# Performance work log

Measured on AMD Instinct MI355X. Metric: run time of the kernel, lower is better.

The kernel has to match this reference:

```python
import jax, jax.numpy as jnp
import numpy as np

B, N, DIM = 2, 2048, 2048
H, KVH, HD = 16, 4, 128
N_REP = H // KVH
SCALE = np.float32(HD ** -0.5)


def setup_inputs() -> dict:
    key = jax.random.key(0)
    ks = jax.random.split(key, 5)
    x = jax.random.normal(ks[0], (B, N, DIM), dtype=jnp.float32)
    mask = jnp.tril(jnp.ones((N, N), dtype=jnp.int32))[None, None]  # [1,1,N,N] causal
    Wq = jax.random.normal(ks[1], (DIM, H * HD), dtype=jnp.float32) * (DIM ** -0.5)
    Wk = jax.random.normal(ks[2], (DIM, KVH * HD), dtype=jnp.float32) * (DIM ** -0.5)
    Wv = jax.random.normal(ks[3], (DIM, KVH * HD), dtype=jnp.float32) * (DIM ** -0.5)
    Wo = jax.random.normal(ks[4], (H * HD, DIM), dtype=jnp.float32) * ((H * HD) ** -0.5)
    return {"x": x, "mask": mask, "Wq": Wq, "Wk": Wk, "Wv": Wv, "Wo": Wo}


def reference(x, mask, Wq, Wk, Wv, Wo):
    Bx, Nx, _ = x.shape
    # projections -> [B, heads, N, head_dim]
    q = (x @ Wq).reshape(Bx, Nx, H, HD).transpose(0, 2, 1, 3)
    k = (x @ Wk).reshape(Bx, Nx, KVH, HD).transpose(0, 2, 1, 3)
    v = (x @ Wv).reshape(Bx, Nx, KVH, HD).transpose(0, 2, 1, 3)
    # repeat_interleave KV heads to match query heads (GQA)
    k = jnp.repeat(k, N_REP, axis=1)
    v = jnp.repeat(v, N_REP, axis=1)
    attn = jnp.einsum('bhqd,bhkd->bhqk', q, k) * SCALE
    attn = jnp.where(mask == 0, jnp.float32(-jnp.inf), attn)
    attn = jax.nn.softmax(attn, axis=-1)
    out = jnp.einsum('bhqk,bhkd->bhqd', attn, v)
    out = out.transpose(0, 2, 1, 3).reshape(Bx, Nx, H * HD)
    return out @ Wo
```

## Files before the change

kernel.cpp:

```cpp
#include <hip/hip_runtime.h>
#include <hip/hip_bf16.h>
#include <math.h>

typedef __bf16 bf16;
typedef bf16 bf16x8 __attribute__((ext_vector_type(8)));
typedef bf16 bf16x4v __attribute__((ext_vector_type(4)));
typedef float f32x4 __attribute__((ext_vector_type(4)));

#define GLD16(g, l) __builtin_amdgcn_global_load_lds(                          \
    (__attribute__((address_space(1))) void*)(g),                              \
    (__attribute__((address_space(3))) void*)(l), 16, 0, 0)

#define MFMA16(a, b, c) __builtin_amdgcn_mfma_f32_16x16x32_bf16((a), (b), (c), 0, 0, 0)

#if __has_builtin(__builtin_amdgcn_exp2f)
#define EXP2F(x) __builtin_amdgcn_exp2f(x)
#else
#define EXP2F(x) exp2f(x)
#endif

__device__ __forceinline__ f32x4 shfl_xor4(f32x4 a, int m) {
  f32x4 r;
  #pragma unroll
  for (int i = 0; i < 4; i++) r[i] = __shfl_xor(a[i], m);
  return r;
}

__global__ __launch_bounds__(256) void prep(const float* __restrict__ x,
                                            const float* __restrict__ Wq,
                                            const float* __restrict__ Wk,
                                            const float* __restrict__ Wv,
                                            const float* __restrict__ Wo,
                                            bf16* __restrict__ Xb,
                                            bf16* __restrict__ Wqkvt,
                                            bf16* __restrict__ Wot,
                                            float qscale) {
  const int id = blockIdx.x;
  const int tid = threadIdx.x;
  if (id >= 10240) {
    int i = (id - 10240) * 256 + tid;
    float4 v = ((const float4*)x)[i];
    bf16x4v o;
    o.x = (bf16)v.x; o.y = (bf16)v.y; o.z = (bf16)v.z; o.w = (bf16)v.w;
    ((bf16x4v*)Xb)[i] = o;
    return;
  }
  __shared__ float t[32][33];
  const float* in; bf16* out; int colsIn, outRowOff, bx, by; float scale;
  if (id < 4096)      { in = Wq; out = Wqkvt; colsIn = 2048; outRowOff = 0;    scale = qscale; bx = id & 63;          by = id >> 6; }
  else if (id < 5120) { in = Wk; out = Wqkvt; colsIn = 512;  outRowOff = 2048; scale = 1.0f;   bx = (id - 4096) & 15; by = (id - 4096) >> 4; }
  else if (id < 6144) { in = Wv; out = Wqkvt; colsIn = 512;  outRowOff = 2560; scale = 1.0f;   bx = (id - 5120) & 15; by = (id - 5120) >> 4; }
  else                { in = Wo; out = Wot;   colsIn = 2048; outRowOff = 0;    scale = 1.0f;   bx = (id - 6144) & 63; by = (id - 6144) >> 6; }
  const int c0 = bx * 32, r0 = by * 32;
  const int tx = tid & 31, ty = tid >> 5;
  #pragma unroll
  for (int i = 0; i < 32; i += 8)
    t[ty + i][tx] = in[(size_t)(r0 + ty + i) * colsIn + (c0 + tx)];
  __syncthreads();
  #pragma unroll
  for (int i = 0; i < 32; i += 8)
    out[(size_t)(outRowOff + c0 + ty + i) * 2048 + (r0 + tx)] = (bf16)(t[tx][ty + i] * scale);
}

__global__ __launch_bounds__(256, 2) void gemm_bt(const bf16* __restrict__ A,
                                                  const bf16* __restrict__ Bt,
                                                  bf16* __restrict__ C,
                                                  bf16* __restrict__ Vg,
                                                  int N, int K) {
  __shared__ __attribute__((aligned(16))) bf16 As[128 * 32];
  __shared__ __attribute__((aligned(16))) bf16 Bs[128 * 32];
  const int tid = threadIdx.x;
  const int lane = tid & 63;
  const int wave = tid >> 6;
  const int wm = wave >> 1, wn = wave & 1;
  const int l15 = lane & 15, quad = lane >> 4;
  const int rowBase = blockIdx.y * 128;
  const int colBase = blockIdx.x * 128;

  f32x4 acc[4][4] = {};

  const int cb0 = wave * 64;
  const int c0 = cb0 + lane;
  const int c1 = c0 + 256;
  const bf16* a0 = A + (size_t)(rowBase + (c0 >> 2)) * K + (c0 & 3) * 8;
  const bf16* a1 = A + (size_t)(rowBase + (c1 >> 2)) * K + (c1 & 3) * 8;
  const bf16* b0 = Bt + (size_t)(colBase + (c0 >> 2)) * K + (c0 & 3) * 8;
  const bf16* b1 = Bt + (size_t)(colBase + (c1 >> 2)) * K + (c1 & 3) * 8;
  bf16* lA0 = &As[cb0 * 8];
  bf16* lA1 = &As[(cb0 + 256) * 8];
  bf16* lB0 = &Bs[cb0 * 8];
  bf16* lB1 = &Bs[(cb0 + 256) * 8];

  for (int k0 = 0; k0 < K; k0 += 32) {
    GLD16(a0 + k0, lA0);
    GLD16(a1 + k0, lA1);
    GLD16(b0 + k0, lB0);
    GLD16(b1 + k0, lB1);
    __syncthreads();
    bf16x8 af[4], bfr[4];
    #pragma unroll
    for (int i = 0; i < 4; i++)
      af[i] = *(const bf16x8*)&As[(wm * 64 + i * 16 + l15) * 32 + quad * 8];
    #pragma unroll
    for (int i = 0; i < 4; i++)
      bfr[i] = *(const bf16x8*)&Bs[(wn * 64 + i * 16 + l15) * 32 + quad * 8];
    #pragma unroll
    for (int i = 0; i < 4; i++)
      #pragma unroll
      for (int j = 0; j < 4; j++)
        acc[i][j] = MFMA16(af[i], bfr[j], acc[i][j]);
    __syncthreads();
  }

  if (colBase >= 2560) {
    const int kvh = (colBase - 2560) >> 7;
    #pragma unroll
    for (int i = 0; i < 4; i++) {
      int row = rowBase + wm * 64 + i * 16 + quad * 4;
      int bb = row >> 11;
      int n0 = row & 2047;
      #pragma unroll
      for (int j = 0; j < 4; j++) {
        int d = wn * 64 + j * 16 + l15;
        bf16x4v o;
        #pragma unroll
        for (int r = 0; r < 4; r++) o[r] = (bf16)acc[i][j][r];
        *(bf16x4v*)&Vg[((size_t)(bb * 4 + kvh) * 128 + d) * 2048 + n0] = o;
      }
    }
  } else {
    #pragma unroll
    for (int i = 0; i < 4; i++) {
      int row = rowBase + wm * 64 + i * 16 + quad * 4;
      #pragma unroll
      for (int j = 0; j < 4; j++) {
        int col = colBase + wn * 64 + j * 16 + l15;
        #pragma unroll
        for (int r = 0; r < 4; r++)
          C[(size_t)(row + r) * N + col] = (bf16)acc[i][j][r];
      }
    }
  }
}

__global__ __launch_bounds__(128, 2) void gemm_bt64(const bf16* __restrict__ A,
                                                    const bf16* __restrict__ Bt,
                                                    float* __restrict__ C,
                                                    int N, int K) {
  __shared__ __attribute__((aligned(16))) bf16 As[64 * 32];
  __shared__ __attribute__((aligned(16))) bf16 Bs[128 * 32];
  const int tid = threadIdx.x;
  const int lane = tid & 63;
  const int wave = tid >> 6;
  const int l15 = lane & 15, quad = lane >> 4;
  const int rowBase = blockIdx.y * 64;
  const int colBase = blockIdx.x * 128;

  f32x4 acc[4][4] = {};

  const bf16* aP[2]; bf16* lAp[2];
  #pragma unroll
  for (int p = 0; p < 2; p++) {
    int s = p * 128 + tid;
    aP[p] = A + (size_t)(rowBase + (s >> 2)) * K + (s & 3) * 8;
    lAp[p] = &As[(p * 128 + wave * 64) * 8];
  }
  const bf16* bP[4]; bf16* lBp[4];
  #pragma unroll
  for (int p = 0; p < 4; p++) {
    int s = p * 128 + tid;
    bP[p] = Bt + (size_t)(colBase + (s >> 2)) * K + (s & 3) * 8;
    lBp[p] = &Bs[(p * 128 + wave * 64) * 8];
  }

  for (int k0 = 0; k0 < K; k0 += 32) {
    #pragma unroll
    for (int p = 0; p < 2; p++) GLD16(aP[p] + k0, lAp[p]);
    #pragma unroll
    for (int p = 0; p < 4; p++) GLD16(bP[p] + k0, lBp[p]);
    __syncthreads();
    bf16x8 af[4], bfr[4];
    #pragma unroll
    for (int i = 0; i < 4; i++)
      af[i] = *(const bf16x8*)&As[(i * 16 + l15) * 32 + quad * 8];
    #pragma unroll
    for (int i = 0; i < 4; i++)
      bfr[i] = *(const bf16x8*)&Bs[(wave * 64 + i * 16 + l15) * 32 + quad * 8];
    #pragma unroll
    for (int i = 0; i < 4; i++)
      #pragma unroll
      for (int j = 0; j < 4; j++)
        acc[i][j] = MFMA16(af[i], bfr[j], acc[i][j]);
    __syncthreads();
  }

  #pragma unroll
  for (int i = 0; i < 4; i++) {
    int row = rowBase + i * 16 + quad * 4;
    #pragma unroll
    for (int j = 0; j < 4; j++) {
      int col = colBase + wave * 64 + j * 16 + l15;
      #pragma unroll
      for (int r = 0; r < 4; r++)
        C[(size_t)(row + r) * N + col] = acc[i][j][r];
    }
  }
}

#define MASKV (-1e30f)

__device__ const unsigned char BMAP[22] = {
  28, 58, 24, 50, 20, 46, 36, 32,
  62, 59, 54, 51, 47, 42, 55, 63,
  0, 4, 8, 12, 16, 43
};

#define SLOT_F32 16640

__global__ __launch_bounds__(256, 2) void gqa_attn(const bf16* __restrict__ QKV,
                                                   const bf16* __restrict__ Vg,
                                                   bf16* __restrict__ Obf,
                                                   float* __restrict__ Part) {
  __shared__ __attribute__((aligned(16))) bf16 Kl[64 * 128];
  __shared__ __attribute__((aligned(16))) bf16 Vt[128 * 64];
  __shared__ __attribute__((aligned(16))) bf16 Pl[4][32 * 68];

  const int tid = threadIdx.x;
  const int lane = tid & 63;
  const int wave = tid >> 6;
  const int l15 = lane & 15, quad = lane >> 4;

  const int e = BMAP[blockIdx.x >> 5];
  const int bh = blockIdx.x & 31;
  const int qt = e >> 2;
  const int split = (e >> 1) & 1;
  const int half = e & 1;
  const int b = bh >> 4, h = bh & 15, kvh = h >> 2;
  const int q0 = qt * 128;
  const int nkt = 2 * qt + 2;
  const int kt_lo = (split && half) ? (nkt >> 1) : 0;
  const int kt_hi = (split && !half) ? (nkt >> 1) : nkt;

  const size_t rs = 3072;
  const bf16* Qb  = QKV + (size_t)b * 2048 * rs + h * 128;
  const bf16* Kb  = QKV + (size_t)b * 2048 * rs + 2048 + kvh * 128;
  const bf16* Vgb = Vg + (size_t)(b * 4 + kvh) * 128 * 2048;

  bf16x8 qf[2][4];
  #pragma unroll
  for (int mt = 0; mt < 2; mt++) {
    int row = q0 + wave * 32 + mt * 16 + l15;
    #pragma unroll
    for (int ks = 0; ks < 4; ks++)
      qf[mt][ks] = *(const bf16x8*)&Qb[(size_t)row * rs + ks * 32 + quad * 8];
  }

  bf16x8 ones8;
  #pragma unroll
  for (int i = 0; i < 8; i++) ones8[i] = (bf16)1.0f;

  const bf16* kp[4]; const bf16* vp[4];
  bf16* kl[4]; bf16* vl[4];
  #pragma unroll
  for (int t = 0; t < 4; t++) {
    int keyl = wave * 16 + t * 4 + (lane >> 4);
    int ck = (lane & 15) ^ (4 * (t & 1) + (lane >> 4));
    kp[t] = Kb + (size_t)(kt_lo * 64 + keyl) * rs + ck * 8;
    kl[t] = &Kl[(wave * 16 + t * 4) * 128];
    int dl = wave * 32 + t * 8 + (lane >> 3);
    int cv = (lane & 7) ^ (lane >> 3);
    vp[t] = Vgb + (size_t)dl * 2048 + kt_lo * 64 + cv * 8;
    vl[t] = &Vt[(wave * 32 + t * 8) * 64];
  }

  f32x4 oacc[2][8] = {};
  f32x4 lacc[2] = {};
  f32x4 mrow[2];
  #pragma unroll
  for (int mt = 0; mt < 2; mt++)
    #pragma unroll
    for (int r = 0; r < 4; r++) mrow[mt][r] = MASKV;

  const int myrow_hi = q0 + wave * 32 + 31;
  for (int kt = kt_lo; kt < kt_hi; kt++) {
    const int k0 = kt * 64;
    __syncthreads();
    #pragma unroll
    for (int t = 0; t < 4; t++) { GLD16(kp[t], kl[t]); kp[t] += 64 * rs; }
    #pragma unroll
    for (int t = 0; t < 4; t++) { GLD16(vp[t], vl[t]); vp[t] += 64; }
    __syncthreads();

    if (k0 > myrow_hi) continue;

    f32x4 s[2][4] = {};
    #pragma unroll
    for (int ks = 0; ks < 4; ks++) {
      #pragma unroll
      for (int nt = 0; nt < 4; nt++) {
        bf16x8 kf = *(const bf16x8*)&Kl[(nt * 16 + l15) * 128 +
                                        (((ks * 4 + quad) ^ (l15 & 7)) * 8)];
        s[0][nt] = MFMA16(qf[0][ks], kf, s[0][nt]);
        s[1][nt] = MFMA16(qf[1][ks], kf, s[1][nt]);
      }
    }
    if (kt >= nkt - 2) {
      #pragma unroll
      for (int mt = 0; mt < 2; mt++) {
        int rowb = q0 + wave * 32 + mt * 16 + quad * 4;
        #pragma unroll
        for (int nt = 0; nt < 4; nt++) {
          int col = k0 + nt * 16 + l15;
          #pragma unroll
          for (int r = 0; r < 4; r++)
            if (col > rowb + r) s[mt][nt][r] = MASKV;
        }
      }
    }
    #pragma unroll
    for (int mt = 0; mt < 2; mt++) {
      f32x4 mx = s[mt][0];
      #pragma unroll
      for (int nt = 1; nt < 4; nt++)
        #pragma unroll
        for (int r = 0; r < 4; r++) mx[r] = fmaxf(mx[r], s[mt][nt][r]);
      #pragma unroll
      for (int d = 1; d < 16; d <<= 1) {
        f32x4 o = shfl_xor4(mx, d);
        #pragma unroll
        for (int r = 0; r < 4; r++) mx[r] = fmaxf(mx[r], o[r]);
      }
      bool noresc = (mx[0] <= mrow[mt][0] + 8.f) && (mx[1] <= mrow[mt][1] + 8.f) &&
                    (mx[2] <= mrow[mt][2] + 8.f) && (mx[3] <= mrow[mt][3] + 8.f);
      if (!__all(noresc)) {
        f32x4 alpha;
        #pragma unroll
        for (int r = 0; r < 4; r++) {
          float mn = fmaxf(mrow[mt][r], mx[r]);
          alpha[r] = EXP2F(mrow[mt][r] - mn);
          mrow[mt][r] = mn;
        }
        #pragma unroll
        for (int no = 0; no < 8; no++)
          #pragma unroll
          for (int r = 0; r < 4; r++) oacc[mt][no][r] *= alpha[r];
        #pragma unroll
        for (int r = 0; r < 4; r++) lacc[mt][r] *= alpha[r];
      }
      #pragma unroll
      for (int nt = 0; nt < 4; nt++)
        #pragma unroll
        for (int r = 0; r < 4; r++) {
          float p = EXP2F(s[mt][nt][r] - mrow[mt][r]);
          Pl[wave][(mt * 16 + quad * 4 + r) * 68 + nt * 16 + l15] = (bf16)p;
        }
    }
    #pragma unroll
    for (int ks2 = 0; ks2 < 2; ks2++) {
      bf16x8 pf0 = *(const bf16x8*)&Pl[wave][l15 * 68 + ks2 * 32 + quad * 8];
      bf16x8 pf1 = *(const bf16x8*)&Pl[wave][(16 + l15) * 68 + ks2 * 32 + quad * 8];
      lacc[0] = MFMA16(pf0, ones8, lacc[0]);
      lacc[1] = MFMA16(pf1, ones8, lacc[1]);
      #pragma unroll
      for (int no = 0; no < 8; no++) {
        bf16x8 vf = *(const bf16x8*)&Vt[(no * 16 + l15) * 64 +
                                        (((ks2 * 4 + quad) ^ (l15 & 7)) * 8)];
        oacc[0][no] = MFMA16(pf0, vf, oacc[0][no]);
        oacc[1][no] = MFMA16(pf1, vf, oacc[1][no]);
      }
    }
  }

  if (!split) {
    #pragma unroll
    for (int mt = 0; mt < 2; mt++) {
      f32x4 linv;
      #pragma unroll
      for (int r = 0; r < 4; r++) linv[r] = 1.0f / lacc[mt][r];
      int row = q0 + wave * 32 + mt * 16 + quad * 4;
      #pragma unroll
      for (int no = 0; no < 8; no++) {
        int col = h * 128 + no * 16 + l15;
        #pragma unroll
        for (int r = 0; r < 4; r++)
          Obf[(size_t)(b * 2048 + row + r) * 2048 + col] = (bf16)(oacc[mt][no][r] * linv[r]);
      }
    }
  } else {
    const int fidx = bh * 6 + (qt - 10);
    float* slot = Part + (size_t)(fidx * 2 + half) * SLOT_F32;
    #pragma unroll
    for (int mt = 0; mt < 2; mt++) {
      int row = wave * 32 + mt * 16 + quad * 4;
      #pragma unroll
      for (int no = 0; no < 8; no++) {
        int col = no * 16 + l15;
        #pragma unroll
        for (int r = 0; r < 4; r++)
          slot[(row + r) * 128 + col] = oacc[mt][no][r];
      }
    }
    if (l15 == 0) {
      #pragma unroll
      for (int mt = 0; mt < 2; mt++)
        #pragma unroll
        for (int r = 0; r < 4; r++) {
          int row = wave * 32 + mt * 16 + quad * 4 + r;
          slot[16384 + row] = mrow[mt][r];
          slot[16512 + row] = lacc[mt][r];
        }
    }
  }
}

__global__ __launch_bounds__(256) void merge_split(const float* __restrict__ Part,
                                                   bf16* __restrict__ Obf) {
  const int fidx = blockIdx.x;
  const int bh = fidx / 6, qt = 10 + fidx % 6;
  const int b = bh >> 4, h = bh & 15;
  const int tid = threadIdx.x;
  const int cl = (tid & 31) * 4;
  const int r0 = tid >> 5;
  const float* s0 = Part + (size_t)(fidx * 2) * SLOT_F32;
  const float* s1 = s0 + SLOT_F32;
  #pragma unroll
  for (int i = 0; i < 16; i++) {
    int row = r0 + i * 8;
    float m0 = s0[16384 + row], l0 = s0[16512 + row];
    float m1 = s1[16384 + row], l1 = s1[16512 + row];
    float ms = fmaxf(m0, m1);
    float a0 = EXP2F(m0 - ms), a1 = EXP2F(m1 - ms);
    float linv = 1.0f / (l0 * a0 + l1 * a1);
    f32x4 v0 = *(const f32x4*)&s0[row * 128 + cl];
    f32x4 v1 = *(const f32x4*)&s1[row * 128 + cl];
    bf16x4v o;
    #pragma unroll
    for (int r = 0; r < 4; r++) o[r] = (bf16)((v0[r] * a0 + v1[r] * a1) * linv);
    *(bf16x4v*)&Obf[(size_t)(b * 2048 + qt * 128 + row) * 2048 + h * 128 + cl] = o;
  }
}

extern "C" void kernel_launch(void* const* d_in, const int* in_sizes, int n_in,
                              void* d_out, int out_size, void* d_ws, size_t ws_size,
                              hipStream_t stream) {
  const float* x  = (const float*)d_in[0];
  const float* Wq = (const float*)d_in[2];
  const float* Wk = (const float*)d_in[3];
  const float* Wv = (const float*)d_in[4];
  const float* Wo = (const float*)d_in[5];
  float* out = (float*)d_out;

  bf16* Xb    = (bf16*)d_ws;
  bf16* Wqkvt = Xb + 8388608;
  bf16* Wot   = Wqkvt + 6291456;
  bf16* QKV   = Wot + 4194304;
  bf16* Obf   = QKV + 12582912;
  bf16* Vg    = Obf + 8388608;

  float* Part = (float*)d_ws;

  const float qscale = (float)(0.08838834764831845 * 1.4426950408889634);

  prep<<<18432, 256, 0, stream>>>(x, Wq, Wk, Wv, Wo, Xb, Wqkvt, Wot, qscale);
  gemm_bt<<<dim3(24, 32), 256, 0, stream>>>(Xb, Wqkvt, QKV, Vg, 3072, 2048);
  gqa_attn<<<704, 256, 0, stream>>>(QKV, Vg, Obf, Part);
  merge_split<<<192, 256, 0, stream>>>(Part, Obf);
  gemm_bt64<<<dim3(16, 64), 128, 0, stream>>>(Obf, Wot, out, 2048, 2048);
}
```

Baseline: 321.1 us.

## Switch attention to transposed 32x32 MFMA with register-resident P via permlane swap

Rewrites the attention inner loop to compute S^T with 32x32x16 MFMAs so each lane owns one query row. Softmax max and sum then need only a single cross-half shuffle, and P is packed to bf16 with v_cvt_pk and redistributed via v_permlane32_swap instead of a round trip through LDS. The row sum is accumulated in VALU rather than by an MFMA against ones, and occupancy is raised to 3 blocks per CU now that the P LDS buffer is gone. The cost is higher register pressure per lane under the tighter launch bound, plus reliance on gfx950-specific instructions.

Result: faster. 303.7 us (-5.4%).

```diff
diff --git a/kernel.cpp b/kernel.cpp
--- a/kernel.cpp
+++ b/kernel.cpp
@@ -6,12 +6,16 @@
 typedef bf16 bf16x8 __attribute__((ext_vector_type(8)));
 typedef bf16 bf16x4v __attribute__((ext_vector_type(4)));
 typedef float f32x4 __attribute__((ext_vector_type(4)));
+typedef float f32x16 __attribute__((ext_vector_type(16)));
+typedef unsigned int u32;
+typedef u32 u32x4 __attribute__((ext_vector_type(4)));
 
 #define GLD16(g, l) __builtin_amdgcn_global_load_lds(                          \
     (__attribute__((address_space(1))) void*)(g),                              \
     (__attribute__((address_space(3))) void*)(l), 16, 0, 0)
 
 #define MFMA16(a, b, c) __builtin_amdgcn_mfma_f32_16x16x32_bf16((a), (b), (c), 0, 0, 0)
+#define MFMA32(a, b, c) __builtin_amdgcn_mfma_f32_32x32x16_bf16((a), (b), (c), 0, 0, 0)
 
 #if __has_builtin(__builtin_amdgcn_exp2f)
 #define EXP2F(x) __builtin_amdgcn_exp2f(x)
@@ -19,11 +23,13 @@
 #define EXP2F(x) exp2f(x)
 #endif
 
-__device__ __forceinline__ f32x4 shfl_xor4(f32x4 a, int m) {
-  f32x4 r;
-  #pragma unroll
-  for (int i = 0; i < 4; i++) r[i] = __shfl_xor(a[i], m);
+__device__ __forceinline__ u32 cvtpk_bf16(float lo, float hi_) {
+  u32 r;
+  asm("v_cvt_pk_bf16_f32 %0, %1, %2" : "=v"(r) : "v"(lo), "v"(hi_));
   return r;
+}
+__device__ __forceinline__ void pl32swap(u32& a, u32& b) {
+  asm("v_permlane32_swap_b32 %0, %1" : "+v"(a), "+v"(b));
 }
 
 __global__ __launch_bounds__(256) void prep(const float* __restrict__ x,
@@ -217,18 +223,17 @@
 
 #define SLOT_F32 16640
 
-__global__ __launch_bounds__(256, 2) void gqa_attn(const bf16* __restrict__ QKV,
+__global__ __launch_bounds__(256, 3) void gqa_attn(const bf16* __restrict__ QKV,
                                                    const bf16* __restrict__ Vg,
                                                    bf16* __restrict__ Obf,
                                                    float* __restrict__ Part) {
   __shared__ __attribute__((aligned(16))) bf16 Kl[64 * 128];
   __shared__ __attribute__((aligned(16))) bf16 Vt[128 * 64];
-  __shared__ __attribute__((aligned(16))) bf16 Pl[4][32 * 68];
 
   const int tid = threadIdx.x;
   const int lane = tid & 63;
   const int wave = tid >> 6;
-  const int l15 = lane & 15, quad = lane >> 4;
+  const int l31 = lane & 31, hi = lane >> 5;
 
   const int e = BMAP[blockIdx.x >> 5];
   const int bh = blockIdx.x & 31;
@@ -246,18 +251,12 @@
   const bf16* Kb  = QKV + (size_t)b * 2048 * rs + 2048 + kvh * 128;
   const bf16* Vgb = Vg + (size_t)(b * 4 + kvh) * 128 * 2048;
 
-  bf16x8 qf[2][4];
-  #pragma unroll
-  for (int mt = 0; mt < 2; mt++) {
-    int row = q0 + wave * 32 + mt * 16 + l15;
-    #pragma unroll
-    for (int ks = 0; ks < 4; ks++)
-      qf[mt][ks] = *(const bf16x8*)&Qb[(size_t)row * rs + ks * 32 + quad * 8];
-  }
-
-  bf16x8 ones8;
-  #pragma unroll
-  for (int i = 0; i < 8; i++) ones8[i] = (bf16)1.0f;
+  const int qrow = q0 + wave * 32 + l31;
+
+  bf16x8 qf[8];
+  #pragma unroll
+  for (int hs = 0; hs < 8; hs++)
+    qf[hs] = *(const bf16x8*)&Qb[(size_t)qrow * rs + hs * 16 + hi * 8];
 
   const bf16* kp[4]; const bf16* vp[4];
   bf16* kl[4]; bf16* vl[4];
@@ -273,13 +272,9 @@
     vl[t] = &Vt[(wave * 32 + t * 8) * 64];
   }
 
-  f32x4 oacc[2][8] = {};
-  f32x4 lacc[2] = {};
-  f32x4 mrow[2];
-  #pragma unroll
-  for (int mt = 0; mt < 2; mt++)
-    #pragma unroll
-    for (int r = 0; r < 4; r++) mrow[mt][r] = MASKV;
+  f32x16 oacc[4] = {};
+  float lacc = 0.f;
+  float mrow = MASKV;
 
   const int myrow_hi = q0 + wave * 32 + 31;
   for (int kt = kt_lo; kt < kt_hi; kt++) {
@@ -293,122 +288,112 @@
 
     if (k0 > myrow_hi) continue;
 
-    f32x4 s[2][4] = {};
+    f32x16 sacc[2] = {};
+    #pragma unroll
+    for (int hs = 0; hs < 8; hs++) {
+      #pragma unroll
+      for (int kg = 0; kg < 2; kg++) {
+        bf16x8 kf = *(const bf16x8*)&Kl[(kg * 32 + l31) * 128 +
+                                        (((hs * 2 + hi) ^ (l31 & 7)) * 8)];
+        sacc[kg] = MFMA32(kf, qf[hs], sacc[kg]);
+      }
+    }
+    if (kt >= nkt - 2) {
+      #pragma unroll
+      for (int kg = 0; kg < 2; kg++)
+        #pragma unroll
+        for (int r = 0; r < 16; r++) {
+          int key = k0 + kg * 32 + (r & 3) + 8 * (r >> 2) + 4 * hi;
+          if (key > qrow) sacc[kg][r] = MASKV;
+        }
+    }
+    float mx = sacc[0][0];
+    #pragma unroll
+    for (int kg = 0; kg < 2; kg++)
+      #pragma unroll
+      for (int r = 0; r < 16; r++) mx = fmaxf(mx, sacc[kg][r]);
+    mx = fmaxf(mx, __shfl_xor(mx, 32));
+    bool noresc = (mx <= mrow + 8.f);
+    if (!__all(noresc)) {
+      float mn = fmaxf(mrow, mx);
+      float alpha = EXP2F(mrow - mn);
+      mrow = mn;
+      #pragma unroll
+      for (int dg = 0; dg < 4; dg++)
+        #pragma unroll
+        for (int r = 0; r < 16; r++) oacc[dg][r] *= alpha;
+      lacc *= alpha;
+    }
+    float ls = 0.f;
+    #pragma unroll
+    for (int kg = 0; kg < 2; kg++)
+      #pragma unroll
+      for (int r = 0; r < 16; r++) {
+        float p = (float)(bf16)EXP2F(sacc[kg][r] - mrow);
+        sacc[kg][r] = p;
+        ls += p;
+      }
+    ls += __shfl_xor(ls, 32);
+    lacc += ls;
+    u32 w[4][4];
+    #pragma unroll
+    for (int kg = 0; kg < 2; kg++) {
+      u32 A0 = cvtpk_bf16(sacc[kg][0], sacc[kg][1]);
+      u32 A1 = cvtpk_bf16(sacc[kg][2], sacc[kg][3]);
+      u32 B0 = cvtpk_bf16(sacc[kg][4], sacc[kg][5]);
+      u32 B1 = cvtpk_bf16(sacc[kg][6], sacc[kg][7]);
+      pl32swap(A0, B0);
+      pl32swap(A1, B1);
+      w[kg * 2][0] = A0; w[kg * 2][1] = A1; w[kg * 2][2] = B0; w[kg * 2][3] = B1;
+      u32 C0 = cvtpk_bf16(sacc[kg][8], sacc[kg][9]);
+      u32 C1 = cvtpk_bf16(sacc[kg][10], sacc[kg][11]);
+      u32 D0 = cvtpk_bf16(sacc[kg][12], sacc[kg][13]);
+      u32 D1 = cvtpk_bf16(sacc[kg][14], sacc[kg][15]);
+      pl32swap(C0, D0);
+      pl32swap(C1, D1);
+      w[kg * 2 + 1][0] = C0; w[kg * 2 + 1][1] = C1; w[kg * 2 + 1][2] = D0; w[kg * 2 + 1][3] = D1;
+    }
     #pragma unroll
     for (int ks = 0; ks < 4; ks++) {
-      #pragma unroll
-      for (int nt = 0; nt < 4; nt++) {
-        bf16x8 kf = *(const bf16x8*)&Kl[(nt * 16 + l15) * 128 +
-                                        (((ks * 4 + quad) ^ (l15 & 7)) * 8)];
-        s[0][nt] = MFMA16(qf[0][ks], kf, s[0][nt]);
-        s[1][nt] = MFMA16(qf[1][ks], kf, s[1][nt]);
-      }
-    }
-    if (kt >= nkt - 2) {
-      #pragma unroll
-      for (int mt = 0; mt < 2; mt++) {
-        int rowb = q0 + wave * 32 + mt * 16 + quad * 4;
-        #pragma unroll
-        for (int nt = 0; nt < 4; nt++) {
-          int col = k0 + nt * 16 + l15;
-          #pragma unroll
-          for (int r = 0; r < 4; r++)
-            if (col > rowb + r) s[mt][nt][r] = MASKV;
-        }
-      }
-    }
-    #pragma unroll
-    for (int mt = 0; mt < 2; mt++) {
-      f32x4 mx = s[mt][0];
-      #pragma unroll
-      for (int nt = 1; nt < 4; nt++)
-        #pragma unroll
-        for (int r = 0; r < 4; r++) mx[r] = fmaxf(mx[r], s[mt][nt][r]);
-      #pragma unroll
-      for (int d = 1; d < 16; d <<= 1) {
-        f32x4 o = shfl_xor4(mx, d);
-        #pragma unroll
-        for (int r = 0; r < 4; r++) mx[r] = fmaxf(mx[r], o[r]);
-      }
-      bool noresc = (mx[0] <= mrow[mt][0] + 8.f) && (mx[1] <= mrow[mt][1] + 8.f) &&
-                    (mx[2] <= mrow[mt][2] + 8.f) && (mx[3] <= mrow[mt][3] + 8.f);
-      if (!__all(noresc)) {
-        f32x4 alpha;
-        #pragma unroll
-        for (int r = 0; r < 4; r++) {
-          float mn = fmaxf(mrow[mt][r], mx[r]);
-          alpha[r] = EXP2F(mrow[mt][r] - mn);
-          mrow[mt][r] = mn;
-        }
-        #pragma unroll
-        for (int no = 0; no < 8; no++)
-          #pragma unroll
-          for (int r = 0; r < 4; r++) oacc[mt][no][r] *= alpha[r];
-        #pragma unroll
-        for (int r = 0; r < 4; r++) lacc[mt][r] *= alpha[r];
-      }
-      #pragma unroll
-      for (int nt = 0; nt < 4; nt++)
-        #pragma unroll
-        for (int r = 0; r < 4; r++) {
-          float p = EXP2F(s[mt][nt][r] - mrow[mt][r]);
-          Pl[wave][(mt * 16 + quad * 4 + r) * 68 + nt * 16 + l15] = (bf16)p;
-        }
-    }
-    #pragma unroll
-    for (int ks2 = 0; ks2 < 2; ks2++) {
-      bf16x8 pf0 = *(const bf16x8*)&Pl[wave][l15 * 68 + ks2 * 32 + quad * 8];
-      bf16x8 pf1 = *(const bf16x8*)&Pl[wave][(16 + l15) * 68 + ks2 * 32 + quad * 8];
-      lacc[0] = MFMA16(pf0, ones8, lacc[0]);
-      lacc[1] = MFMA16(pf1, ones8, lacc[1]);
-      #pragma unroll
-      for (int no = 0; no < 8; no++) {
-        bf16x8 vf = *(const bf16x8*)&Vt[(no * 16 + l15) * 64 +
-                                        (((ks2 * 4 + quad) ^ (l15 & 7)) * 8)];
-        oacc[0][no] = MFMA16(pf0, vf, oacc[0][no]);
-        oacc[1][no] = MFMA16(pf1, vf, oacc[1][no]);
+      u32x4 pw = {w[ks][0], w[ks][1], w[ks][2], w[ks][3]};
+      bf16x8 pb = __builtin_bit_cast(bf16x8, pw);
+      #pragma unroll
+      for (int dg = 0; dg < 4; dg++) {
+        bf16x8 va = *(const bf16x8*)&Vt[(dg * 32 + l31) * 64 +
+                                        (((ks * 2 + hi) ^ (l31 & 7)) * 8)];
+        oacc[dg] = MFMA32(va, pb, oacc[dg]);
       }
     }
   }
 
   if (!split) {
-    #pragma unroll
-    for (int mt = 0; mt < 2; mt++) {
-      f32x4 linv;
-      #pragma unroll
-      for (int r = 0; r < 4; r++) linv[r] = 1.0f / lacc[mt][r];
-      int row = q0 + wave * 32 + mt * 16 + quad * 4;
-      #pragma unroll
-      for (int no = 0; no < 8; no++) {
-        int col = h * 128 + no * 16 + l15;
-        #pragma unroll
-        for (int r = 0; r < 4; r++)
-          Obf[(size_t)(b * 2048 + row + r) * 2048 + col] = (bf16)(oacc[mt][no][r] * linv[r]);
-      }
-    }
+    float linv = 1.0f / lacc;
+    const size_t orow = (size_t)(b * 2048 + qrow) * 2048 + h * 128;
+    #pragma unroll
+    for (int dg = 0; dg < 4; dg++)
+      #pragma unroll
+      for (int rq = 0; rq < 4; rq++) {
+        bf16x4v o;
+        #pragma unroll
+        for (int j = 0; j < 4; j++) o[j] = (bf16)(oacc[dg][rq * 4 + j] * linv);
+        *(bf16x4v*)&Obf[orow + dg * 32 + rq * 8 + hi * 4] = o;
+      }
   } else {
     const int fidx = bh * 6 + (qt - 10);
     float* slot = Part + (size_t)(fidx * 2 + half) * SLOT_F32;
-    #pragma unroll
-    for (int mt = 0; mt < 2; mt++) {
-      int row = wave * 32 + mt * 16 + quad * 4;
-      #pragma unroll
-      for (int no = 0; no < 8; no++) {
-        int col = no * 16 + l15;
-        #pragma unroll
-        for (int r = 0; r < 4; r++)
-          slot[(row + r) * 128 + col] = oacc[mt][no][r];
-      }
-    }
-    if (l15 == 0) {
-      #pragma unroll
-      for (int mt = 0; mt < 2; mt++)
-        #pragma unroll
-        for (int r = 0; r < 4; r++) {
-          int row = wave * 32 + mt * 16 + quad * 4 + r;
-          slot[16384 + row] = mrow[mt][r];
-          slot[16512 + row] = lacc[mt][r];
-        }
+    const int rl = wave * 32 + l31;
+    #pragma unroll
+    for (int dg = 0; dg < 4; dg++)
+      #pragma unroll
+      for (int rq = 0; rq < 4; rq++) {
+        f32x4 o4;
+        #pragma unroll
+        for (int j = 0; j < 4; j++) o4[j] = oacc[dg][rq * 4 + j];
+        *(f32x4*)&slot[rl * 128 + dg * 32 + rq * 8 + hi * 4] = o4;
+      }
+    if (hi == 0) {
+      slot[16384 + rl] = mrow;
+      slot[16512 + rl] = lacc;
     }
   }
 }
```
